# Kernel tuning notes

Hardware: AMD Instinct MI355X
Metric: run time of the kernel (lower is better)

## Reference

```python
import jax, jax.numpy as jnp
import numpy as np

EPS = 1e-6
N_HEADS = 16
KV_HEADS = 4
HEAD_DIM = 64
N_REP = N_HEADS // KV_HEADS
N_EXPERTS = 8
TOP_K = 2


def _rms_norm(x, w):
    return x * jax.lax.rsqrt(jnp.mean(x * x, axis=-1, keepdims=True) + EPS) * w


def _apply_rope(x, fc):
    # x: (B,T,H,D); fc: (T, D//2, 2) holding (cos, sin)
    B, T, H, D = x.shape
    xr = x.reshape(B, T, H, D // 2, 2)
    f = fc.reshape(1, T, 1, D // 2, 2)
    re = xr[..., 0] * f[..., 0] - xr[..., 1] * f[..., 1]
    im = xr[..., 1] * f[..., 0] + xr[..., 0] * f[..., 1]
    return jnp.stack([re, im], axis=-1).reshape(B, T, H, D)


def _silu(x):
    return x * jax.nn.sigmoid(x)


def setup_inputs():
    key = jax.random.key(0)
    ks = jax.random.split(key, 16)
    B, T, C = 4, 1024, 1024
    IE, IS = 1024, 2048  # expert_inter_dim, shared inter_dim
    s = 0.02
    x = jax.random.normal(ks[0], (B, T, C), jnp.float32)
    inv_freq = 1.0 / (10000.0 ** (np.arange(0, HEAD_DIM, 2, dtype=np.float32) / HEAD_DIM))
    ang = np.outer(np.arange(T, dtype=np.float32), inv_freq)
    freq_cis = jnp.asarray(np.stack([np.cos(ang), np.sin(ang)], axis=-1), jnp.float32)
    causal = np.tril(np.ones((T, T), dtype=bool))
    mask = jnp.asarray(np.where(causal, 0.0, -1e9), dtype=jnp.float32).reshape(1, 1, T, T)
    window = jnp.zeros((1, 1, T, T), jnp.float32)
    return {
        "x": x,
        "freq_cis": freq_cis,
        "mask": mask,
        "window": window,
        "norm1_w": jnp.ones((C,), jnp.float32),
        "wq": jax.random.normal(ks[1], (N_HEADS * HEAD_DIM, C), jnp.float32) * s,
        "wk": jax.random.normal(ks[2], (KV_HEADS * HEAD_DIM, C), jnp.float32) * s,
        "wv": jax.random.normal(ks[3], (KV_HEADS * HEAD_DIM, C), jnp.float32) * s,
        "wo": jax.random.normal(ks[4], (C, N_HEADS * HEAD_DIM), jnp.float32) * s,
        "norm2_w": jnp.ones((C,), jnp.float32),
        "gate_w": jax.random.normal(ks[5], (N_EXPERTS, C), jnp.float32) * s,
        "exp_w1": jax.random.normal(ks[6], (N_EXPERTS, IE, C), jnp.float32) * s,
        "exp_w2": jax.random.normal(ks[7], (N_EXPERTS, IE, C), jnp.float32) * s,
        "exp_wp": jax.random.normal(ks[8], (N_EXPERTS, C, IE), jnp.float32) * s,
        "sh_w1": jax.random.normal(ks[9], (IS, C), jnp.float32) * s,
        "sh_w2": jax.random.normal(ks[10], (IS, C), jnp.float32) * s,
        "sh_wp": jax.random.normal(ks[11], (C, IS), jnp.float32) * s,
        "start_pos": 0,
    }


def reference(x, freq_cis, mask, window, norm1_w, wq, wk, wv, wo, norm2_w,
              gate_w, exp_w1, exp_w2, exp_wp, sh_w1, sh_w2, sh_wp, start_pos):
    B, T, C = x.shape
    # ---- pre-norm attention (GQA, Global mask, eval: no dropout) ----
    xn = _rms_norm(x, norm1_w)
    q = (xn @ wq.T).reshape(B, T, N_HEADS, HEAD_DIM)
    k = (xn @ wk.T).reshape(B, T, KV_HEADS, HEAD_DIM)
    v = (xn @ wv.T).reshape(B, T, KV_HEADS, HEAD_DIM)
    q = _apply_rope(q, freq_cis)
    k = _apply_rope(k, freq_cis)
    k = jnp.repeat(k, N_REP, axis=2)  # (B,T,H,D)
    v = jnp.repeat(v, N_REP, axis=2)
    scale = 1.0 / np.sqrt(HEAD_DIM).astype(np.float32)
    att = jnp.einsum("bqhd,bkhd->bhqk", q, k) * scale + mask
    p = jax.nn.softmax(att, axis=-1)
    o = jnp.einsum("bhqk,bkhd->bqhd", p, v).reshape(B, T, C)
    x = x + o @ wo.T
    # ---- pre-norm MoE FFN ----
    xn2 = _rms_norm(x, norm2_w).reshape(-1, C)  # (N,C)
    scores = xn2 @ gate_w.T                      # gate logits, returned
    probs = jax.nn.softmax(scores, axis=-1)
    top_w, top_i = jax.lax.top_k(probs, TOP_K)   # (N,K)
    # dense combine weights (N,E): zero for non-selected experts
    wfull = jnp.sum(jax.nn.one_hot(top_i, N_EXPERTS, dtype=x.dtype) * top_w[..., None], axis=1)
    h = _silu(jnp.einsum("nc,eic->eni", xn2, exp_w1)) * jnp.einsum("nc,eic->eni", xn2, exp_w2)
    ye = jnp.einsum("eni,eci->enc", h, exp_wp)   # per-expert outputs
    y = jnp.einsum("ne,enc->nc", wfull, ye)      # routed combine
    z = (_silu(xn2 @ sh_w1.T) * (xn2 @ sh_w2.T)) @ sh_wp.T  # shared expert
    out = x + (y + z).reshape(B, T, C)
    return out, scores
```

## Files before the change

### kernel.cpp

```cpp
#include <hip/hip_runtime.h>


typedef __bf16 bf16_t;
typedef __bf16 bf16x8 __attribute__((ext_vector_type(8)));
typedef __bf16 bf16x4 __attribute__((ext_vector_type(4)));
typedef float  f32x4  __attribute__((ext_vector_type(4)));

#define GLD16(gp, lp) __builtin_amdgcn_global_load_lds(                         \
    (const __attribute__((address_space(1))) void*)(gp),                        \
    (__attribute__((address_space(3))) void*)(lp), 16, 0, 0)

__global__ __launch_bounds__(256) void convert_k(
    const float* __restrict__ src, bf16_t* __restrict__ dst)
{
    size_t i = (size_t)blockIdx.x * 256 + threadIdx.x;
    float4 v = *((const float4*)src + i);
    bf16x4 o;
    o[0] = (bf16_t)v.x; o[1] = (bf16_t)v.y; o[2] = (bf16_t)v.z; o[3] = (bf16_t)v.w;
    *((bf16x4*)dst + i) = o;
}

__global__ __launch_bounds__(256) void gemm_bt(
    const bf16_t* __restrict__ A, const bf16_t* __restrict__ W,
    int M, int N, int K, int ldw, int mode,
    float* __restrict__ outF, bf16_t* __restrict__ outB,
    const float* __restrict__ resF)
{
    __shared__ __align__(16) bf16_t sA[128 * 64];
    __shared__ __align__(16) bf16_t sB[128 * 64];
    const int tid  = threadIdx.x;
    const int bm   = blockIdx.y * 128, bn = blockIdx.x * 128;
    const int lane = tid & 63;
    const int wv   = tid >> 6;
    const int wm   = (wv >> 1) * 64, wn = (wv & 1) * 64;
    const int lr   = lane & 15;
    const int kg   = lane >> 4;

    f32x4 acc[4][4];
    #pragma unroll
    for (int i = 0; i < 4; ++i)
        #pragma unroll
        for (int j = 0; j < 4; ++j)
            acc[i][j] = f32x4{0.f, 0.f, 0.f, 0.f};

    for (int k0 = 0; k0 < K; k0 += 64) {
        #pragma unroll
        for (int p = 0; p < 4; ++p) {
            int idx = p * 256 + tid;
            int row = idx >> 3, ch = (idx & 7) * 8;
            GLD16(A + (size_t)(bm + row) * K   + k0 + ch, sA + idx * 8);
            GLD16(W + (size_t)(bn + row) * ldw + k0 + ch, sB + idx * 8);
        }
        __syncthreads();
        #pragma unroll
        for (int ks = 0; ks < 2; ++ks) {
            bf16x8 af[4], bfr[4];
            #pragma unroll
            for (int i = 0; i < 4; ++i)
                af[i] = *(const bf16x8*)(sA + (wm + i * 16 + lr) * 64 + ks * 32 + kg * 8);
            #pragma unroll
            for (int j = 0; j < 4; ++j)
                bfr[j] = *(const bf16x8*)(sB + (wn + j * 16 + lr) * 64 + ks * 32 + kg * 8);
            #pragma unroll
            for (int i = 0; i < 4; ++i)
                #pragma unroll
                for (int j = 0; j < 4; ++j)
                    acc[i][j] = __builtin_amdgcn_mfma_f32_16x16x32_bf16(
                        af[i], bfr[j], acc[i][j], 0, 0, 0);
        }
        __syncthreads();
    }

    #pragma unroll
    for (int i = 0; i < 4; ++i) {
        #pragma unroll
        for (int j = 0; j < 4; ++j) {
            #pragma unroll
            for (int rr = 0; rr < 4; ++rr) {
                int m = bm + wm + i * 16 + kg * 4 + rr;
                int n = bn + wn + j * 16 + lr;
                size_t o = (size_t)m * N + n;
                float v = acc[i][j][rr];
                if (mode == 0)      outF[o] = v;
                else if (mode == 1) outB[o] = (bf16_t)v;
                else                outF[o] = v + resF[o];
            }
        }
    }
}

__global__ __launch_bounds__(256) void gemm_glu(
    const bf16_t* __restrict__ A, const bf16_t* __restrict__ W1,
    const bf16_t* __restrict__ W2, int M, int N, int K,
    bf16_t* __restrict__ out)
{
    __shared__ __align__(16) bf16_t sA[128 * 64];
    __shared__ __align__(16) bf16_t sB1[128 * 64];
    __shared__ __align__(16) bf16_t sB2[128 * 64];
    const int tid  = threadIdx.x;
    const int bm   = blockIdx.y * 128, bn = blockIdx.x * 128;
    const int lane = tid & 63;
    const int wv   = tid >> 6;
    const int wm   = (wv >> 1) * 64, wn = (wv & 1) * 64;
    const int lr   = lane & 15;
    const int kg   = lane >> 4;

    f32x4 acc1[4][4], acc2[4][4];
    #pragma unroll
    for (int i = 0; i < 4; ++i)
        #pragma unroll
        for (int j = 0; j < 4; ++j) {
            acc1[i][j] = f32x4{0.f, 0.f, 0.f, 0.f};
            acc2[i][j] = f32x4{0.f, 0.f, 0.f, 0.f};
        }

    for (int k0 = 0; k0 < K; k0 += 64) {
        #pragma unroll
        for (int p = 0; p < 4; ++p) {
            int idx = p * 256 + tid;
            int row = idx >> 3, ch = (idx & 7) * 8;
            GLD16(A  + (size_t)(bm + row) * K + k0 + ch, sA  + idx * 8);
            GLD16(W1 + (size_t)(bn + row) * K + k0 + ch, sB1 + idx * 8);
            GLD16(W2 + (size_t)(bn + row) * K + k0 + ch, sB2 + idx * 8);
        }
        __syncthreads();
        #pragma unroll
        for (int ks = 0; ks < 2; ++ks) {
            bf16x8 af[4], b1[4], b2[4];
            #pragma unroll
            for (int i = 0; i < 4; ++i)
                af[i] = *(const bf16x8*)(sA + (wm + i * 16 + lr) * 64 + ks * 32 + kg * 8);
            #pragma unroll
            for (int j = 0; j < 4; ++j) {
                b1[j] = *(const bf16x8*)(sB1 + (wn + j * 16 + lr) * 64 + ks * 32 + kg * 8);
                b2[j] = *(const bf16x8*)(sB2 + (wn + j * 16 + lr) * 64 + ks * 32 + kg * 8);
            }
            #pragma unroll
            for (int i = 0; i < 4; ++i)
                #pragma unroll
                for (int j = 0; j < 4; ++j) {
                    acc1[i][j] = __builtin_amdgcn_mfma_f32_16x16x32_bf16(
                        af[i], b1[j], acc1[i][j], 0, 0, 0);
                    acc2[i][j] = __builtin_amdgcn_mfma_f32_16x16x32_bf16(
                        af[i], b2[j], acc2[i][j], 0, 0, 0);
                }
        }
        __syncthreads();
    }

    #pragma unroll
    for (int i = 0; i < 4; ++i) {
        #pragma unroll
        for (int j = 0; j < 4; ++j) {
            #pragma unroll
            for (int rr = 0; rr < 4; ++rr) {
                int m = bm + wm + i * 16 + kg * 4 + rr;
                int n = bn + wn + j * 16 + lr;
                float v1 = acc1[i][j][rr], v2 = acc2[i][j][rr];
                out[(size_t)m * N + n] = (bf16_t)(v1 / (1.f + __expf(-v1)) * v2);
            }
        }
    }
}

__global__ __launch_bounds__(256) void glu_gather(
    const bf16_t* __restrict__ A, const bf16_t* __restrict__ W1,
    const bf16_t* __restrict__ W2, const int* __restrict__ tok_list,
    const int* __restrict__ cnt, const int* __restrict__ off,
    bf16_t* __restrict__ h)
{
    const int e = blockIdx.y >> 5, t = blockIdx.y & 31;
    const int ce = cnt[e];
    if (t * 128 >= ce) return;
    const int hbase = off[e] + t * 128;
    const bf16_t* W1e = W1 + (size_t)e * 1048576;
    const bf16_t* W2e = W2 + (size_t)e * 1048576;

    __shared__ __align__(16) bf16_t sA[128 * 64];
    __shared__ __align__(16) bf16_t sB1[128 * 64];
    __shared__ __align__(16) bf16_t sB2[128 * 64];
    const int tid  = threadIdx.x;
    const int bn   = blockIdx.x * 128;
    const int lane = tid & 63;
    const int wv   = tid >> 6;
    const int wm   = (wv >> 1) * 64, wn = (wv & 1) * 64;
    const int lr   = lane & 15;
    const int kg   = lane >> 4;

    int tok4[4];
    #pragma unroll
    for (int p = 0; p < 4; ++p)
        tok4[p] = tok_list[e * 4096 + t * 128 + p * 32 + (tid >> 3)];

    f32x4 acc1[4][4], acc2[4][4];
    #pragma unroll
    for (int i = 0; i < 4; ++i)
        #pragma unroll
        for (int j = 0; j < 4; ++j) {
            acc1[i][j] = f32x4{0.f, 0.f, 0.f, 0.f};
            acc2[i][j] = f32x4{0.f, 0.f, 0.f, 0.f};
        }

    for (int k0 = 0; k0 < 1024; k0 += 64) {
        #pragma unroll
        for (int p = 0; p < 4; ++p) {
            int idx = p * 256 + tid;
            int row = idx >> 3, ch = (idx & 7) * 8;
            GLD16(A   + (size_t)tok4[p] * 1024 + k0 + ch, sA  + idx * 8);
            GLD16(W1e + (size_t)(bn + row) * 1024 + k0 + ch, sB1 + idx * 8);
            GLD16(W2e + (size_t)(bn + row) * 1024 + k0 + ch, sB2 + idx * 8);
        }
        __syncthreads();
        #pragma unroll
        for (int ks = 0; ks < 2; ++ks) {
            bf16x8 af[4], b1[4], b2[4];
            #pragma unroll
            for (int i = 0; i < 4; ++i)
                af[i] = *(const bf16x8*)(sA + (wm + i * 16 + lr) * 64 + ks * 32 + kg * 8);
            #pragma unroll
            for (int j = 0; j < 4; ++j) {
                b1[j] = *(const bf16x8*)(sB1 + (wn + j * 16 + lr) * 64 + ks * 32 + kg * 8);
                b2[j] = *(const bf16x8*)(sB2 + (wn + j * 16 + lr) * 64 + ks * 32 + kg * 8);
            }
            #pragma unroll
            for (int i = 0; i < 4; ++i)
                #pragma unroll
                for (int j = 0; j < 4; ++j) {
                    acc1[i][j] = __builtin_amdgcn_mfma_f32_16x16x32_bf16(
                        af[i], b1[j], acc1[i][j], 0, 0, 0);
                    acc2[i][j] = __builtin_amdgcn_mfma_f32_16x16x32_bf16(
                        af[i], b2[j], acc2[i][j], 0, 0, 0);
                }
        }
        __syncthreads();
    }

    #pragma unroll
    for (int i = 0; i < 4; ++i) {
        #pragma unroll
        for (int j = 0; j < 4; ++j) {
            #pragma unroll
            for (int rr = 0; rr < 4; ++rr) {
                int rl = wm + i * 16 + kg * 4 + rr;
                int n  = bn + wn + j * 16 + lr;
                float v1 = acc1[i][j][rr], v2 = acc2[i][j][rr];
                h[(size_t)(hbase + rl) * 1024 + n] =
                    (bf16_t)(v1 / (1.f + __expf(-v1)) * v2);
            }
        }
    }
}

__global__ __launch_bounds__(256) void down_gather(
    const bf16_t* __restrict__ h, const bf16_t* __restrict__ Wp,
    const int* __restrict__ tok_list, const float* __restrict__ w_list,
    const int* __restrict__ cnt, const int* __restrict__ off,
    float* __restrict__ y)
{
    const int e = blockIdx.y >> 5, t = blockIdx.y & 31;
    const int ce = cnt[e];
    if (t * 128 >= ce) return;
    const int hbase = off[e] + t * 128;
    const bf16_t* We = Wp + (size_t)e * 1048576;

    __shared__ __align__(16) bf16_t sA[128 * 64];
    __shared__ __align__(16) bf16_t sB[128 * 64];
    const int tid  = threadIdx.x;
    const int bn   = blockIdx.x * 128;
    const int lane = tid & 63;
    const int wv   = tid >> 6;
    const int wm   = (wv >> 1) * 64, wn = (wv & 1) * 64;
    const int lr   = lane & 15;
    const int kg   = lane >> 4;

    f32x4 acc[4][4];
    #pragma unroll
    for (int i = 0; i < 4; ++i)
        #pragma unroll
        for (int j = 0; j < 4; ++j)
            acc[i][j] = f32x4{0.f, 0.f, 0.f, 0.f};

    for (int k0 = 0; k0 < 1024; k0 += 64) {
        #pragma unroll
        for (int p = 0; p < 4; ++p) {
            int idx = p * 256 + tid;
            int row = idx >> 3, ch = (idx & 7) * 8;
            GLD16(h  + (size_t)(hbase + row) * 1024 + k0 + ch, sA + idx * 8);
            GLD16(We + (size_t)(bn + row) * 1024 + k0 + ch,    sB + idx * 8);
        }
        __syncthreads();
        #pragma unroll
        for (int ks = 0; ks < 2; ++ks) {
            bf16x8 af[4], bfr[4];
            #pragma unroll
            for (int i = 0; i < 4; ++i)
                af[i] = *(const bf16x8*)(sA + (wm + i * 16 + lr) * 64 + ks * 32 + kg * 8);
            #pragma unroll
            for (int j = 0; j < 4; ++j)
                bfr[j] = *(const bf16x8*)(sB + (wn + j * 16 + lr) * 64 + ks * 32 + kg * 8);
            #pragma unroll
            for (int i = 0; i < 4; ++i)
                #pragma unroll
                for (int j = 0; j < 4; ++j)
                    acc[i][j] = __builtin_amdgcn_mfma_f32_16x16x32_bf16(
                        af[i], bfr[j], acc[i][j], 0, 0, 0);
        }
        __syncthreads();
    }

    #pragma unroll
    for (int i = 0; i < 4; ++i) {
        #pragma unroll
        for (int rr = 0; rr < 4; ++rr) {
            int rl = t * 128 + wm + i * 16 + kg * 4 + rr;
            if (rl < ce) {
                int   tok = tok_list[e * 4096 + rl];
                float wgt = w_list[e * 4096 + rl];
                #pragma unroll
                for (int j = 0; j < 4; ++j) {
                    int n = bn + wn + j * 16 + lr;
                    atomicAdd(&y[(size_t)tok * 1024 + n], wgt * acc[i][j][rr]);
                }
            }
        }
    }
}

__global__ __launch_bounds__(256) void rmsnorm_k(
    const float* __restrict__ src, const float* __restrict__ w,
    bf16_t* __restrict__ dst)
{
    const int row = blockIdx.x, tid = threadIdx.x;
    float4 t4 = *((const float4*)src + (size_t)row * 256 + tid);
    float ssum = t4.x*t4.x + t4.y*t4.y + t4.z*t4.z + t4.w*t4.w;
    #pragma unroll
    for (int off = 32; off > 0; off >>= 1) ssum += __shfl_down(ssum, off);
    __shared__ float red[4];
    if ((tid & 63) == 0) red[tid >> 6] = ssum;
    __syncthreads();
    float total = red[0] + red[1] + red[2] + red[3];
    float rms = rsqrtf(total * (1.0f / 1024.0f) + 1e-6f);
    float4 w4 = *((const float4*)w + tid);
    bf16x4 o4;
    o4[0] = (bf16_t)(t4.x * rms * w4.x);
    o4[1] = (bf16_t)(t4.y * rms * w4.y);
    o4[2] = (bf16_t)(t4.z * rms * w4.z);
    o4[3] = (bf16_t)(t4.w * rms * w4.w);
    *((bf16x4*)dst + (size_t)row * 256 + tid) = o4;
}

__global__ __launch_bounds__(256) void rmsnorm_gate_k(
    const float* __restrict__ src, const float* __restrict__ w,
    const float* __restrict__ gw, bf16_t* __restrict__ dst,
    float* __restrict__ scores, int* __restrict__ topi,
    float* __restrict__ topw)
{
    const int row = blockIdx.x, tid = threadIdx.x;
    float4 t4 = *((const float4*)src + (size_t)row * 256 + tid);
    float ssum = t4.x*t4.x + t4.y*t4.y + t4.z*t4.z + t4.w*t4.w;
    #pragma unroll
    for (int off = 32; off > 0; off >>= 1) ssum += __shfl_down(ssum, off);
    __shared__ float red[4];
    if ((tid & 63) == 0) red[tid >> 6] = ssum;
    __syncthreads();
    float total = red[0] + red[1] + red[2] + red[3];
    float rms = rsqrtf(total * (1.0f / 1024.0f) + 1e-6f);
    float4 w4 = *((const float4*)w + tid);
    float4 f4;
    f4.x = t4.x * rms * w4.x;
    f4.y = t4.y * rms * w4.y;
    f4.z = t4.z * rms * w4.z;
    f4.w = t4.w * rms * w4.w;
    bf16x4 o4;
    o4[0] = (bf16_t)f4.x; o4[1] = (bf16_t)f4.y;
    o4[2] = (bf16_t)f4.z; o4[3] = (bf16_t)f4.w;
    *((bf16x4*)dst + (size_t)row * 256 + tid) = o4;

    float a[8];
    #pragma unroll
    for (int e = 0; e < 8; ++e) {
        float4 g4 = *((const float4*)(gw + (size_t)e * 1024) + tid);
        a[e] = f4.x * g4.x + f4.y * g4.y + f4.z * g4.z + f4.w * g4.w;
    }
    #pragma unroll
    for (int e = 0; e < 8; ++e)
        #pragma unroll
        for (int off = 32; off > 0; off >>= 1) a[e] += __shfl_down(a[e], off);
    __shared__ float gred[4][8];
    if ((tid & 63) == 0)
        #pragma unroll
        for (int e = 0; e < 8; ++e) gred[tid >> 6][e] = a[e];
    __syncthreads();
    if (tid == 0) {
        float lg[8];
        #pragma unroll
        for (int e = 0; e < 8; ++e)
            lg[e] = gred[0][e] + gred[1][e] + gred[2][e] + gred[3][e];
        #pragma unroll
        for (int e = 0; e < 8; ++e) scores[(size_t)row * 8 + e] = lg[e];
        float mx = lg[0];
        #pragma unroll
        for (int e = 1; e < 8; ++e) mx = fmaxf(mx, lg[e]);
        float p[8], sum = 0.f;
        #pragma unroll
        for (int e = 0; e < 8; ++e) { p[e] = __expf(lg[e] - mx); sum += p[e]; }
        float inv = 1.0f / sum;
        #pragma unroll
        for (int e = 0; e < 8; ++e) p[e] *= inv;
        int i1 = 0;
        #pragma unroll
        for (int e = 1; e < 8; ++e) if (p[e] > p[i1]) i1 = e;
        int i2 = (i1 == 0) ? 1 : 0;
        #pragma unroll
        for (int e = 0; e < 8; ++e) if (e != i1 && p[e] > p[i2]) i2 = e;
        topi[row] = i1 | (i2 << 8);
        topw[row * 2]     = p[i1];
        topw[row * 2 + 1] = p[i2];
    }
}

__global__ __launch_bounds__(256) void build_lists_k(
    const int* __restrict__ topi, const float* __restrict__ topw,
    int* __restrict__ tok_list, float* __restrict__ w_list,
    int* __restrict__ cnt)
{
    const int e = blockIdx.x;
    const int tid = threadIdx.x, lane = tid & 63, wv = tid >> 6;
    __shared__ int wc[4];
    int base = 0;
    for (int t0 = 0; t0 < 4096; t0 += 256) {
        int tok = t0 + tid;
        int ti = topi[tok];
        int i1 = ti & 255, i2 = (ti >> 8) & 255;
        bool m = (i1 == e) || (i2 == e);
        unsigned long long b = __ballot(m);
        if (lane == 0) wc[wv] = __popcll(b);
        __syncthreads();
        int pos = base;
        #pragma unroll
        for (int k = 0; k < 4; ++k) if (k < wv) pos += wc[k];
        pos += __popcll(b & ((1ull << lane) - 1ull));
        if (m) {
            tok_list[e * 4096 + pos] = tok;
            w_list[e * 4096 + pos]   = (i1 == e) ? topw[tok * 2] : topw[tok * 2 + 1];
        }
        base += wc[0] + wc[1] + wc[2] + wc[3];
        __syncthreads();
    }
    int padded = (base + 127) & ~127;
    for (int p = base + tid; p < padded; p += 256) tok_list[e * 4096 + p] = 0;
    if (tid == 0) cnt[e] = base;
}

__global__ void plan_k(const int* __restrict__ cnt, int* __restrict__ off)
{
    if (threadIdx.x == 0) {
        int run = 0;
        for (int e = 0; e < 8; ++e) {
            off[e] = run;
            run += (cnt[e] + 127) & ~127;
        }
    }
}

__global__ __launch_bounds__(256) void rope_k(
    bf16_t* __restrict__ buf, const float* __restrict__ fc, int nh)
{
    int idx = blockIdx.x * 256 + threadIdx.x;
    int pr = idx & 31;
    int hn = idx >> 5;
    int h  = hn % nh;
    int n  = hn / nh;
    int tpos = n & 1023;
    const float* f = fc + ((size_t)tpos * 32 + pr) * 2;
    float c = f[0], s = f[1];
    size_t base = ((size_t)n * nh + h) * 64 + pr * 2;
    float x0 = (float)buf[base], x1 = (float)buf[base + 1];
    buf[base]     = (bf16_t)(x0 * c - x1 * s);
    buf[base + 1] = (bf16_t)(x1 * c + x0 * s);
}

__global__ __launch_bounds__(256) void transpose_v(
    const bf16_t* __restrict__ vb, bf16_t* __restrict__ vt)
{
    __shared__ bf16_t tile[64][72];
    const int tt = blockIdx.x, kvh = blockIdx.y, b = blockIdx.z;
    const int tid = threadIdx.x;
    {
        int r = tid >> 2, c = (tid & 3) * 16;
        const bf16_t* src = vb + ((size_t)(b * 1024 + tt * 64 + r)) * 256 + kvh * 64 + c;
        bf16x8 v0 = *(const bf16x8*)src;
        bf16x8 v1 = *(const bf16x8*)(src + 8);
        *(bf16x8*)&tile[r][c] = v0;
        *(bf16x8*)&tile[r][c + 8] = v1;
    }
    __syncthreads();
    {
        int d = tid >> 2, t4 = (tid & 3) * 16;
        bf16_t* dst = vt + ((size_t)((b * 4 + kvh) * 64 + d)) * 1024 + tt * 64 + t4;
        bf16x8 o0, o1;
        #pragma unroll
        for (int u = 0; u < 8; ++u) {
            o0[u] = tile[t4 + u][d];
            o1[u] = tile[t4 + 8 + u][d];
        }
        *(bf16x8*)dst = o0;
        *(bf16x8*)(dst + 8) = o1;
    }
}

__global__ __launch_bounds__(256) void attn_mfma(
    const bf16_t* __restrict__ qb, const bf16_t* __restrict__ kb,
    const bf16_t* __restrict__ vt, bf16_t* __restrict__ ob)
{
    const int qt = blockIdx.x, h = blockIdx.y, b = blockIdx.z;
    const int kvh = h >> 2;
    __shared__ __align__(16) bf16_t sK[64 * 64];
    __shared__ __align__(16) bf16_t sVt[64 * 64];
    __shared__ __align__(16) bf16_t sP[64 * 72];
    const int tid  = threadIdx.x;
    const int w    = tid >> 6;
    const int lane = tid & 63;
    const int lr   = lane & 15;
    const int kg   = lane >> 4;

    bf16x8 qf[2];
    {
        const bf16_t* qrow = qb + ((size_t)(b * 1024 + qt * 64 + w * 16 + lr)) * 1024 + h * 64;
        qf[0] = *(const bf16x8*)(qrow + kg * 8);
        qf[1] = *(const bf16x8*)(qrow + 32 + kg * 8);
    }
    float m_run[4], l_run[4];
    f32x4 o_acc[4];
    #pragma unroll
    for (int rr = 0; rr < 4; ++rr) { m_run[rr] = -1.0e30f; l_run[rr] = 0.f; }
    #pragma unroll
    for (int dt = 0; dt < 4; ++dt) o_acc[dt] = f32x4{0.f, 0.f, 0.f, 0.f};

    for (int kt = 0; kt <= qt; ++kt) {
        #pragma unroll
        for (int p = 0; p < 2; ++p) {
            int idx = p * 256 + tid;
            int row = idx >> 3, ch = (idx & 7) * 8;
            GLD16(kb + ((size_t)(b * 1024 + kt * 64 + row)) * 256 + kvh * 64 + ch,
                  sK + idx * 8);
            GLD16(vt + ((size_t)((b * 4 + kvh) * 64 + row)) * 1024 + kt * 64 + ch,
                  sVt + idx * 8);
        }
        __syncthreads();

        f32x4 sfr[4];
        #pragma unroll
        for (int j = 0; j < 4; ++j) {
            sfr[j] = f32x4{0.f, 0.f, 0.f, 0.f};
            #pragma unroll
            for (int ks = 0; ks < 2; ++ks) {
                bf16x8 bf = *(const bf16x8*)(sK + (j * 16 + lr) * 64 + ks * 32 + kg * 8);
                sfr[j] = __builtin_amdgcn_mfma_f32_16x16x32_bf16(qf[ks], bf, sfr[j], 0, 0, 0);
            }
        }
        const int rowg = qt * 64 + w * 16 + kg * 4;
        float mnew[4];
        #pragma unroll
        for (int rr = 0; rr < 4; ++rr) mnew[rr] = m_run[rr];
        #pragma unroll
        for (int j = 0; j < 4; ++j) {
            int colg = kt * 64 + j * 16 + lr;
            #pragma unroll
            for (int rr = 0; rr < 4; ++rr) {
                float s = sfr[j][rr] * 0.125f;
                if (colg > rowg + rr) s = -1.0e30f;
                sfr[j][rr] = s;
                mnew[rr] = fmaxf(mnew[rr], s);
            }
        }
        #pragma unroll
        for (int off = 1; off < 16; off <<= 1)
            #pragma unroll
            for (int rr = 0; rr < 4; ++rr)
                mnew[rr] = fmaxf(mnew[rr], __shfl_xor(mnew[rr], off, 64));
        float alpha[4], lpart[4];
        #pragma unroll
        for (int rr = 0; rr < 4; ++rr) {
            alpha[rr] = __expf(m_run[rr] - mnew[rr]);
            lpart[rr] = 0.f;
        }
        #pragma unroll
        for (int j = 0; j < 4; ++j)
            #pragma unroll
            for (int rr = 0; rr < 4; ++rr) {
                float p = __expf(sfr[j][rr] - mnew[rr]);
                sfr[j][rr] = p;
                lpart[rr] += p;
            }
        #pragma unroll
        for (int j = 0; j < 4; ++j)
            #pragma unroll
            for (int rr = 0; rr < 4; ++rr)
                sP[(w * 16 + kg * 4 + rr) * 72 + j * 16 + lr] = (bf16_t)sfr[j][rr];
        #pragma unroll
        for (int off = 1; off < 16; off <<= 1)
            #pragma unroll
            for (int rr = 0; rr < 4; ++rr)
                lpart[rr] += __shfl_xor(lpart[rr], off, 64);
        #pragma unroll
        for (int rr = 0; rr < 4; ++rr) {
            l_run[rr] = l_run[rr] * alpha[rr] + lpart[rr];
            m_run[rr] = mnew[rr];
        }
        #pragma unroll
        for (int dt = 0; dt < 4; ++dt)
            #pragma unroll
            for (int rr = 0; rr < 4; ++rr)
                o_acc[dt][rr] *= alpha[rr];
        #pragma unroll
        for (int ks = 0; ks < 2; ++ks) {
            bf16x8 af = *(const bf16x8*)(sP + (w * 16 + lr) * 72 + ks * 32 + kg * 8);
            #pragma unroll
            for (int dt = 0; dt < 4; ++dt) {
                bf16x8 bf = *(const bf16x8*)(sVt + (dt * 16 + lr) * 64 + ks * 32 + kg * 8);
                o_acc[dt] = __builtin_amdgcn_mfma_f32_16x16x32_bf16(af, bf, o_acc[dt], 0, 0, 0);
            }
        }
        __syncthreads();
    }

    float inv[4];
    #pragma unroll
    for (int rr = 0; rr < 4; ++rr) inv[rr] = 1.0f / l_run[rr];
    #pragma unroll
    for (int dt = 0; dt < 4; ++dt)
        #pragma unroll
        for (int rr = 0; rr < 4; ++rr) {
            int tok = qt * 64 + w * 16 + kg * 4 + rr;
            ob[((size_t)(b * 1024 + tok)) * 1024 + h * 64 + dt * 16 + lr] =
                (bf16_t)(o_acc[dt][rr] * inv[rr]);
        }
}

__global__ __launch_bounds__(256) void finalize_k(
    const float* __restrict__ x1, const float* __restrict__ y, float* __restrict__ out)
{
    size_t i = (size_t)blockIdx.x * 256 + threadIdx.x;
    float4 a = *((const float4*)x1 + i);
    float4 b = *((const float4*)y + i);
    float4 o4;
    o4.x = a.x + b.x; o4.y = a.y + b.y; o4.z = a.z + b.z; o4.w = a.w + b.w;
    *((float4*)out + i) = o4;
}

extern "C" void kernel_launch(void* const* d_in, const int* in_sizes, int n_in,
                              void* d_out, int out_size, void* d_ws, size_t ws_size,
                              hipStream_t stream)
{
    const float* x   = (const float*)d_in[0];
    const float* fc  = (const float*)d_in[1];
    const float* n1w = (const float*)d_in[4];
    const float* wq  = (const float*)d_in[5];
    const float* wk  = (const float*)d_in[6];
    const float* wv  = (const float*)d_in[7];
    const float* wo  = (const float*)d_in[8];
    const float* n2w = (const float*)d_in[9];
    const float* gw  = (const float*)d_in[10];
    const float* ew1 = (const float*)d_in[11];
    const float* ew2 = (const float*)d_in[12];
    const float* ewp = (const float*)d_in[13];
    const float* sw1 = (const float*)d_in[14];
    const float* sw2 = (const float*)d_in[15];
    const float* swp = (const float*)d_in[16];

    const size_t MB = 1024 * 1024;
    char* ws = (char*)d_ws;
    bf16_t* xnb  = (bf16_t*)(ws + 0);
    float*  x1   = (float*) (ws + 8 * MB);
    float*  y    = (float*) (ws + 24 * MB);
    char*   slotA= ws + 40 * MB;
    bf16_t* h    = (bf16_t*)(ws + 56 * MB);
    char*   lists= ws + 74 * MB;
    int*    tok_list = (int*)lists;
    float*  w_list   = (float*)(lists + 131072);
    int*    cnt      = (int*)(lists + 262144);
    int*    off      = (int*)(lists + 262208);
    int*    topi     = (int*)(lists + 262400);
    float*  topw     = (float*)(lists + 278784);
    bf16_t* qb   = (bf16_t*)(ws + 75 * MB);
    bf16_t* kb   = (bf16_t*)(ws + 83 * MB);
    bf16_t* vb   = (bf16_t*)(ws + 85 * MB);
    bf16_t* ob   = (bf16_t*)(ws + 87 * MB);
    bf16_t* vt   = (bf16_t*)(ws + 95 * MB);

    float* outp   = (float*)d_out;
    float* scores = outp + (size_t)4096 * 1024;

    auto conv = [&](const float* s, bf16_t* d, size_t cntN) {
        convert_k<<<cntN / 1024, 256, 0, stream>>>(s, d);
    };
    auto gemm = [&](const bf16_t* A, const bf16_t* W, int M, int N, int K, int ldw,
                    int mode, float* oF, bf16_t* oB, const float* res) {
        gemm_bt<<<dim3(N / 128, M / 128), 256, 0, stream>>>(
            A, W, M, N, K, ldw, mode, oF, oB, res);
    };
    auto glu = [&](const bf16_t* A, const bf16_t* W1, const bf16_t* W2,
                   int M, int N, int K, bf16_t* o) {
        gemm_glu<<<dim3(N / 128, M / 128), 256, 0, stream>>>(A, W1, W2, M, N, K, o);
    };

    bf16_t* wqb = (bf16_t*)slotA;
    bf16_t* wkb = wqb + 1048576;
    bf16_t* wvb = wkb + 262144;
    bf16_t* wob = wvb + 262144;
    conv(wq, wqb, 1048576);
    conv(wk, wkb, 262144);
    conv(wv, wvb, 262144);
    conv(wo, wob, 1048576);

    rmsnorm_k<<<4096, 256, 0, stream>>>(x, n1w, xnb);
    gemm(xnb, wqb, 4096, 1024, 1024, 1024, 1, nullptr, qb, nullptr);
    gemm(xnb, wkb, 4096, 256, 1024, 1024, 1, nullptr, kb, nullptr);
    gemm(xnb, wvb, 4096, 256, 1024, 1024, 1, nullptr, vb, nullptr);
    rope_k<<<(4096 * 16 * 32) / 256, 256, 0, stream>>>(qb, fc, 16);
    rope_k<<<(4096 * 4 * 32) / 256, 256, 0, stream>>>(kb, fc, 4);
    transpose_v<<<dim3(16, 4, 4), 256, 0, stream>>>(vb, vt);
    attn_mfma<<<dim3(16, 16, 4), 256, 0, stream>>>(qb, kb, vt, ob);
    gemm(ob, wob, 4096, 1024, 1024, 1024, 2, x1, nullptr, x);

    rmsnorm_gate_k<<<4096, 256, 0, stream>>>(x1, n2w, gw, xnb, scores, topi, topw);
    build_lists_k<<<8, 256, 0, stream>>>(topi, topw, tok_list, w_list, cnt);
    plan_k<<<1, 64, 0, stream>>>(cnt, off);

    bf16_t* sw1b = (bf16_t*)(ws + 75 * MB);
    bf16_t* sw2b = sw1b + 2097152;
    bf16_t* swpb = sw2b + 2097152;
    conv(sw1, sw1b, 2097152);
    conv(sw2, sw2b, 2097152);
    conv(swp, swpb, 2097152);
    bf16_t* hb = (bf16_t*)slotA;
    glu(xnb, sw1b, sw2b, 4096, 2048, 1024, hb);
    gemm(hb, swpb, 4096, 1024, 2048, 2048, 0, y, nullptr, nullptr);

    bf16_t* ew1b = (bf16_t*)slotA;
    bf16_t* ew2b = (bf16_t*)(ws + 75 * MB);
    conv(ew1, ew1b, 8388608);
    conv(ew2, ew2b, 8388608);
    glu_gather<<<dim3(8, 256), 256, 0, stream>>>(xnb, ew1b, ew2b,
                                                 tok_list, cnt, off, h);
    bf16_t* ewpb = (bf16_t*)slotA;
    conv(ewp, ewpb, 8388608);
    down_gather<<<dim3(8, 256), 256, 0, stream>>>(h, ewpb,
                                                  tok_list, w_list, cnt, off, y);

    finalize_k<<<(4096 * 1024) / 1024, 256, 0, stream>>>(x1, y, outp);
    (void)in_sizes; (void)n_in; (void)out_size; (void)ws_size;
}
```

Baseline: 740.7 us.

## Fuse QKV projection, batch weight conversions, accumulate MoE outputs directly into output

Merges the Q/K/V projections into one GEMM over a packed QKV buffer and applies RoPE to Q and K in one kernel. Weight conversions are batched into multi-segment launches, and the plan and finalize kernels are removed by computing segment offsets inline and accumulating shared and routed expert outputs directly into the output. It also adds an XOR swizzle for K/V tiles in attention LDS to reduce bank conflicts. The risk lies in workspace aliasing and reliance on launch ordering.

```diff
diff --git a/kernel.cpp b/kernel.cpp
--- a/kernel.cpp
+++ b/kernel.cpp
@@ -5,6 +5,8 @@
 typedef __bf16 bf16x8 __attribute__((ext_vector_type(8)));
 typedef __bf16 bf16x4 __attribute__((ext_vector_type(4)));
 typedef float  f32x4  __attribute__((ext_vector_type(4)));
+
+#define LQKV 1536
 
 #define GLD16(gp, lp) __builtin_amdgcn_global_load_lds(                         \
     (const __attribute__((address_space(1))) void*)(gp),                        \
@@ -20,11 +22,30 @@
     *((bf16x4*)dst + i) = o;
 }
 
+struct Cvt8 {
+    const float* s[8];
+    bf16_t* d[8];
+    int cum[9];
+    int nseg;
+};
+
+__global__ __launch_bounds__(256) void convert_multi_k(Cvt8 j)
+{
+    int blk = blockIdx.x;
+    int seg = 0;
+    while (seg + 1 < j.nseg && blk >= j.cum[seg + 1]) ++seg;
+    size_t i = (size_t)(blk - j.cum[seg]) * 256 + threadIdx.x;
+    float4 v = *((const float4*)j.s[seg] + i);
+    bf16x4 o;
+    o[0] = (bf16_t)v.x; o[1] = (bf16_t)v.y; o[2] = (bf16_t)v.z; o[3] = (bf16_t)v.w;
+    *((bf16x4*)j.d[seg] + i) = o;
+}
+
 __global__ __launch_bounds__(256) void gemm_bt(
     const bf16_t* __restrict__ A, const bf16_t* __restrict__ W,
     int M, int N, int K, int ldw, int mode,
     float* __restrict__ outF, bf16_t* __restrict__ outB,
-    const float* __restrict__ resF)
+    const float* __restrict__ resF, float* __restrict__ outF2)
 {
     __shared__ __align__(16) bf16_t sA[128 * 64];
     __shared__ __align__(16) bf16_t sB[128 * 64];
@@ -83,7 +104,11 @@
                 float v = acc[i][j][rr];
                 if (mode == 0)      outF[o] = v;
                 else if (mode == 1) outB[o] = (bf16_t)v;
-                else                outF[o] = v + resF[o];
+                else if (mode == 2) {
+                    float r = v + resF[o];
+                    outF[o] = r;
+                    if (outF2) outF2[o] = r;
+                } else              outF[o] += v;
             }
         }
     }
@@ -163,16 +188,23 @@
     }
 }
 
+__device__ __forceinline__ int seg_off(const int* cnt, int e)
+{
+    int r = 0;
+    #pragma unroll
+    for (int k = 0; k < 8; ++k) if (k < e) r += (cnt[k] + 127) & ~127;
+    return r;
+}
+
 __global__ __launch_bounds__(256) void glu_gather(
     const bf16_t* __restrict__ A, const bf16_t* __restrict__ W1,
     const bf16_t* __restrict__ W2, const int* __restrict__ tok_list,
-    const int* __restrict__ cnt, const int* __restrict__ off,
-    bf16_t* __restrict__ h)
+    const int* __restrict__ cnt, bf16_t* __restrict__ h)
 {
     const int e = blockIdx.y >> 5, t = blockIdx.y & 31;
     const int ce = cnt[e];
     if (t * 128 >= ce) return;
-    const int hbase = off[e] + t * 128;
+    const int hbase = seg_off(cnt, e) + t * 128;
     const bf16_t* W1e = W1 + (size_t)e * 1048576;
     const bf16_t* W2e = W2 + (size_t)e * 1048576;
 
@@ -190,7 +222,7 @@
     int tok4[4];
     #pragma unroll
     for (int p = 0; p < 4; ++p)
-        tok4[p] = tok_list[e * 4096 + t * 128 + p * 32 + (tid >> 3)];
+        tok4[p] = tok_list[e * 4096 + t * 128 + ((p * 256 + tid) >> 3)];
 
     f32x4 acc1[4][4], acc2[4][4];
     #pragma unroll
@@ -206,7 +238,7 @@
         for (int p = 0; p < 4; ++p) {
             int idx = p * 256 + tid;
             int row = idx >> 3, ch = (idx & 7) * 8;
-            GLD16(A   + (size_t)tok4[p] * 1024 + k0 + ch, sA  + idx * 8);
+            GLD16(A   + (size_t)tok4[p] * 1024 + k0 + ch,    sA  + idx * 8);
             GLD16(W1e + (size_t)(bn + row) * 1024 + k0 + ch, sB1 + idx * 8);
             GLD16(W2e + (size_t)(bn + row) * 1024 + k0 + ch, sB2 + idx * 8);
         }
@@ -254,13 +286,12 @@
 __global__ __launch_bounds__(256) void down_gather(
     const bf16_t* __restrict__ h, const bf16_t* __restrict__ Wp,
     const int* __restrict__ tok_list, const float* __restrict__ w_list,
-    const int* __restrict__ cnt, const int* __restrict__ off,
-    float* __restrict__ y)
+    const int* __restrict__ cnt, float* __restrict__ out)
 {
     const int e = blockIdx.y >> 5, t = blockIdx.y & 31;
     const int ce = cnt[e];
     if (t * 128 >= ce) return;
-    const int hbase = off[e] + t * 128;
+    const int hbase = seg_off(cnt, e) + t * 128;
     const bf16_t* We = Wp + (size_t)e * 1048576;
 
     __shared__ __align__(16) bf16_t sA[128 * 64];
@@ -312,14 +343,14 @@
     for (int i = 0; i < 4; ++i) {
         #pragma unroll
         for (int rr = 0; rr < 4; ++rr) {
-            int rl = t * 128 + wm + i * 16 + kg * 4 + rr;
-            if (rl < ce) {
-                int   tok = tok_list[e * 4096 + rl];
-                float wgt = w_list[e * 4096 + rl];
+            int g = t * 128 + wm + i * 16 + kg * 4 + rr;
+            if (g < ce) {
+                int   tok = tok_list[e * 4096 + g];
+                float wgt = w_list[e * 4096 + g];
                 #pragma unroll
                 for (int j = 0; j < 4; ++j) {
                     int n = bn + wn + j * 16 + lr;
-                    atomicAdd(&y[(size_t)tok * 1024 + n], wgt * acc[i][j][rr]);
+                    atomicAdd(&out[(size_t)tok * 1024 + n], wgt * acc[i][j][rr]);
                 }
             }
         }
@@ -452,43 +483,34 @@
     if (tid == 0) cnt[e] = base;
 }
 
-__global__ void plan_k(const int* __restrict__ cnt, int* __restrict__ off)
-{
-    if (threadIdx.x == 0) {
-        int run = 0;
-        for (int e = 0; e < 8; ++e) {
-            off[e] = run;
-            run += (cnt[e] + 127) & ~127;
-        }
-    }
-}
-
-__global__ __launch_bounds__(256) void rope_k(
-    bf16_t* __restrict__ buf, const float* __restrict__ fc, int nh)
+__global__ __launch_bounds__(256) void rope_all_k(
+    bf16_t* __restrict__ qkv, const float* __restrict__ fc)
 {
     int idx = blockIdx.x * 256 + threadIdx.x;
     int pr = idx & 31;
     int hn = idx >> 5;
-    int h  = hn % nh;
-    int n  = hn / nh;
+    int h  = hn % 20;
+    int n  = hn / 20;
     int tpos = n & 1023;
     const float* f = fc + ((size_t)tpos * 32 + pr) * 2;
     float c = f[0], s = f[1];
-    size_t base = ((size_t)n * nh + h) * 64 + pr * 2;
-    float x0 = (float)buf[base], x1 = (float)buf[base + 1];
-    buf[base]     = (bf16_t)(x0 * c - x1 * s);
-    buf[base + 1] = (bf16_t)(x1 * c + x0 * s);
+    int col = (h < 16) ? h * 64 : 1024 + (h - 16) * 64;
+    size_t base = (size_t)n * LQKV + col + pr * 2;
+    float x0 = (float)qkv[base], x1 = (float)qkv[base + 1];
+    qkv[base]     = (bf16_t)(x0 * c - x1 * s);
+    qkv[base + 1] = (bf16_t)(x1 * c + x0 * s);
 }
 
 __global__ __launch_bounds__(256) void transpose_v(
-    const bf16_t* __restrict__ vb, bf16_t* __restrict__ vt)
+    const bf16_t* __restrict__ qkv, bf16_t* __restrict__ vt)
 {
     __shared__ bf16_t tile[64][72];
     const int tt = blockIdx.x, kvh = blockIdx.y, b = blockIdx.z;
     const int tid = threadIdx.x;
     {
         int r = tid >> 2, c = (tid & 3) * 16;
-        const bf16_t* src = vb + ((size_t)(b * 1024 + tt * 64 + r)) * 256 + kvh * 64 + c;
+        const bf16_t* src = qkv + ((size_t)(b * 1024 + tt * 64 + r)) * LQKV
+                            + 1280 + kvh * 64 + c;
         bf16x8 v0 = *(const bf16x8*)src;
         bf16x8 v1 = *(const bf16x8*)(src + 8);
         *(bf16x8*)&tile[r][c] = v0;
@@ -510,8 +532,8 @@
 }
 
 __global__ __launch_bounds__(256) void attn_mfma(
-    const bf16_t* __restrict__ qb, const bf16_t* __restrict__ kb,
-    const bf16_t* __restrict__ vt, bf16_t* __restrict__ ob)
+    const bf16_t* __restrict__ qkv, const bf16_t* __restrict__ vt,
+    bf16_t* __restrict__ ob)
 {
     const int qt = blockIdx.x, h = blockIdx.y, b = blockIdx.z;
     const int kvh = h >> 2;
@@ -523,10 +545,12 @@
     const int lane = tid & 63;
     const int lr   = lane & 15;
     const int kg   = lane >> 4;
+    const int swz  = (lr & 7) << 3;
 
     bf16x8 qf[2];
     {
-        const bf16_t* qrow = qb + ((size_t)(b * 1024 + qt * 64 + w * 16 + lr)) * 1024 + h * 64;
+        const bf16_t* qrow = qkv + ((size_t)(b * 1024 + qt * 64 + w * 16 + lr)) * LQKV
+                             + h * 64;
         qf[0] = *(const bf16x8*)(qrow + kg * 8);
         qf[1] = *(const bf16x8*)(qrow + 32 + kg * 8);
     }
@@ -541,10 +565,11 @@
         #pragma unroll
         for (int p = 0; p < 2; ++p) {
             int idx = p * 256 + tid;
-            int row = idx >> 3, ch = (idx & 7) * 8;
-            GLD16(kb + ((size_t)(b * 1024 + kt * 64 + row)) * 256 + kvh * 64 + ch,
-                  sK + idx * 8);
-            GLD16(vt + ((size_t)((b * 4 + kvh) * 64 + row)) * 1024 + kt * 64 + ch,
+            int row = idx >> 3;
+            int chs = ((idx & 7) * 8) ^ ((row & 7) << 3);
+            GLD16(qkv + ((size_t)(b * 1024 + kt * 64 + row)) * LQKV
+                      + 1024 + kvh * 64 + chs, sK + idx * 8);
+            GLD16(vt + ((size_t)((b * 4 + kvh) * 64 + row)) * 1024 + kt * 64 + chs,
                   sVt + idx * 8);
         }
         __syncthreads();
@@ -555,7 +580,8 @@
             sfr[j] = f32x4{0.f, 0.f, 0.f, 0.f};
             #pragma unroll
             for (int ks = 0; ks < 2; ++ks) {
-                bf16x8 bf = *(const bf16x8*)(sK + (j * 16 + lr) * 64 + ks * 32 + kg * 8);
+                bf16x8 bf = *(const bf16x8*)(sK + (j * 16 + lr) * 64 +
+                                             ((ks * 32 + kg * 8) ^ swz));
                 sfr[j] = __builtin_amdgcn_mfma_f32_16x16x32_bf16(qf[ks], bf, sfr[j], 0, 0, 0);
             }
         }
@@ -618,7 +644,8 @@
             bf16x8 af = *(const bf16x8*)(sP + (w * 16 + lr) * 72 + ks * 32 + kg * 8);
             #pragma unroll
             for (int dt = 0; dt < 4; ++dt) {
-                bf16x8 bf = *(const bf16x8*)(sVt + (dt * 16 + lr) * 64 + ks * 32 + kg * 8);
+                bf16x8 bf = *(const bf16x8*)(sVt + (dt * 16 + lr) * 64 +
+                                             ((ks * 32 + kg * 8) ^ swz));
                 o_acc[dt] = __builtin_amdgcn_mfma_f32_16x16x32_bf16(af, bf, o_acc[dt], 0, 0, 0);
             }
         }
@@ -636,17 +663,6 @@
             ob[((size_t)(b * 1024 + tok)) * 1024 + h * 64 + dt * 16 + lr] =
                 (bf16_t)(o_acc[dt][rr] * inv[rr]);
         }
-}
-
-__global__ __launch_bounds__(256) void finalize_k(
-    const float* __restrict__ x1, const float* __restrict__ y, float* __restrict__ out)
-{
-    size_t i = (size_t)blockIdx.x * 256 + threadIdx.x;
-    float4 a = *((const float4*)x1 + i);
-    float4 b = *((const float4*)y + i);
-    float4 o4;
-    o4.x = a.x + b.x; o4.y = a.y + b.y; o4.z = a.z + b.z; o4.w = a.w + b.w;
-    *((float4*)out + i) = o4;
 }
 
 extern "C" void kernel_launch(void* const* d_in, const int* in_sizes, int n_in,
@@ -673,82 +689,79 @@
     char* ws = (char*)d_ws;
     bf16_t* xnb  = (bf16_t*)(ws + 0);
     float*  x1   = (float*) (ws + 8 * MB);
-    float*  y    = (float*) (ws + 24 * MB);
-    char*   slotA= ws + 40 * MB;
-    bf16_t* h    = (bf16_t*)(ws + 56 * MB);
-    char*   lists= ws + 74 * MB;
+    bf16_t* ew2b = (bf16_t*)(ws + 8 * MB);
+    bf16_t* h    = (bf16_t*)(ws + 24 * MB);
+    char*   lists= ws + 42 * MB;
     int*    tok_list = (int*)lists;
     float*  w_list   = (float*)(lists + 131072);
     int*    cnt      = (int*)(lists + 262144);
-    int*    off      = (int*)(lists + 262208);
     int*    topi     = (int*)(lists + 262400);
     float*  topw     = (float*)(lists + 278784);
-    bf16_t* qb   = (bf16_t*)(ws + 75 * MB);
-    bf16_t* kb   = (bf16_t*)(ws + 83 * MB);
-    bf16_t* vb   = (bf16_t*)(ws + 85 * MB);
-    bf16_t* ob   = (bf16_t*)(ws + 87 * MB);
-    bf16_t* vt   = (bf16_t*)(ws + 95 * MB);
+    bf16_t* sw1b = (bf16_t*)(ws + 43 * MB);
+    bf16_t* sw2b = (bf16_t*)(ws + 47 * MB);
+    bf16_t* swpb = (bf16_t*)(ws + 51 * MB);
+    char*   slotA= ws + 55 * MB;
+    bf16_t* hb   = (bf16_t*)slotA;
+    bf16_t* qkv  = (bf16_t*)(ws + 71 * MB);
+    bf16_t* ob   = (bf16_t*)(ws + 83 * MB);
+    bf16_t* vt   = (bf16_t*)(ws + 91 * MB);
+    bf16_t* ew1b = (bf16_t*)(ws + 71 * MB);
+    bf16_t* ewpb = (bf16_t*)(ws + 71 * MB);
 
     float* outp   = (float*)d_out;
     float* scores = outp + (size_t)4096 * 1024;
 
-    auto conv = [&](const float* s, bf16_t* d, size_t cntN) {
-        convert_k<<<cntN / 1024, 256, 0, stream>>>(s, d);
-    };
     auto gemm = [&](const bf16_t* A, const bf16_t* W, int M, int N, int K, int ldw,
-                    int mode, float* oF, bf16_t* oB, const float* res) {
+                    int mode, float* oF, bf16_t* oB, const float* res, float* oF2) {
         gemm_bt<<<dim3(N / 128, M / 128), 256, 0, stream>>>(
-            A, W, M, N, K, ldw, mode, oF, oB, res);
-    };
-    auto glu = [&](const bf16_t* A, const bf16_t* W1, const bf16_t* W2,
-                   int M, int N, int K, bf16_t* o) {
-        gemm_glu<<<dim3(N / 128, M / 128), 256, 0, stream>>>(A, W1, W2, M, N, K, o);
+            A, W, M, N, K, ldw, mode, oF, oB, res, oF2);
     };
 
     bf16_t* wqb = (bf16_t*)slotA;
     bf16_t* wkb = wqb + 1048576;
     bf16_t* wvb = wkb + 262144;
     bf16_t* wob = wvb + 262144;
-    conv(wq, wqb, 1048576);
-    conv(wk, wkb, 262144);
-    conv(wv, wvb, 262144);
-    conv(wo, wob, 1048576);
+    {
+        Cvt8 j;
+        j.s[0]=wq;  j.d[0]=wqb;  j.s[1]=wk;  j.d[1]=wkb;
+        j.s[2]=wv;  j.d[2]=wvb;  j.s[3]=wo;  j.d[3]=wob;
+        j.s[4]=sw1; j.d[4]=sw1b; j.s[5]=sw2; j.d[5]=sw2b;
+        j.s[6]=swp; j.d[6]=swpb; j.s[7]=nullptr; j.d[7]=nullptr;
+        int sz[7] = {1024, 256, 256, 1024, 2048, 2048, 2048};
+        j.cum[0] = 0;
+        for (int k = 0; k < 7; ++k) j.cum[k + 1] = j.cum[k] + sz[k];
+        j.cum[8] = j.cum[7];
+        j.nseg = 7;
+        convert_multi_k<<<j.cum[7], 256, 0, stream>>>(j);
+    }
 
     rmsnorm_k<<<4096, 256, 0, stream>>>(x, n1w, xnb);
-    gemm(xnb, wqb, 4096, 1024, 1024, 1024, 1, nullptr, qb, nullptr);
-    gemm(xnb, wkb, 4096, 256, 1024, 1024, 1, nullptr, kb, nullptr);
-    gemm(xnb, wvb, 4096, 256, 1024, 1024, 1, nullptr, vb, nullptr);
-    rope_k<<<(4096 * 16 * 32) / 256, 256, 0, stream>>>(qb, fc, 16);
-    rope_k<<<(4096 * 4 * 32) / 256, 256, 0, stream>>>(kb, fc, 4);
-    transpose_v<<<dim3(16, 4, 4), 256, 0, stream>>>(vb, vt);
-    attn_mfma<<<dim3(16, 16, 4), 256, 0, stream>>>(qb, kb, vt, ob);
-    gemm(ob, wob, 4096, 1024, 1024, 1024, 2, x1, nullptr, x);
+    gemm(xnb, wqb, 4096, LQKV, 1024, 1024, 1, nullptr, qkv, nullptr, nullptr);
+    rope_all_k<<<(4096 * 20 * 32) / 256, 256, 0, stream>>>(qkv, fc);
+    transpose_v<<<dim3(16, 4, 4), 256, 0, stream>>>(qkv, vt);
+    attn_mfma<<<dim3(16, 16, 4), 256, 0, stream>>>(qkv, vt, ob);
+    gemm(ob, wob, 4096, 1024, 1024, 1024, 2, x1, nullptr, x, outp);
 
     rmsnorm_gate_k<<<4096, 256, 0, stream>>>(x1, n2w, gw, xnb, scores, topi, topw);
     build_lists_k<<<8, 256, 0, stream>>>(topi, topw, tok_list, w_list, cnt);
-    plan_k<<<1, 64, 0, stream>>>(cnt, off);
-
-    bf16_t* sw1b = (bf16_t*)(ws + 75 * MB);
-    bf16_t* sw2b = sw1b + 2097152;
-    bf16_t* swpb = sw2b + 2097152;
-    conv(sw1, sw1b, 2097152);
-    conv(sw2, sw2b, 2097152);
-    conv(swp, swpb, 2097152);
-    bf16_t* hb = (bf16_t*)slotA;
-    glu(xnb, sw1b, sw2b, 4096, 2048, 1024, hb);
-    gemm(hb, swpb, 4096, 1024, 2048, 2048, 0, y, nullptr, nullptr);
-
-    bf16_t* ew1b = (bf16_t*)slotA;
-    bf16_t* ew2b = (bf16_t*)(ws + 75 * MB);
-    conv(ew1, ew1b, 8388608);
-    conv(ew2, ew2b, 8388608);
-    glu_gather<<<dim3(8, 256), 256, 0, stream>>>(xnb, ew1b, ew2b,
-                                                 tok_list, cnt, off, h);
-    bf16_t* ewpb = (bf16_t*)slotA;
-    conv(ewp, ewpb, 8388608);
-    down_gather<<<dim3(8, 256), 256, 0, stream>>>(h, ewpb,
-                                                  tok_list, w_list, cnt, off, y);
-
-    finalize_k<<<(4096 * 1024) / 1024, 256, 0, stream>>>(x1, y, outp);
+
+    {
+        Cvt8 j;
+        j.s[0]=ew1; j.d[0]=ew1b; j.s[1]=ew2; j.d[1]=ew2b;
+        for (int k = 2; k < 8; ++k) { j.s[k]=nullptr; j.d[k]=nullptr; }
+        j.cum[0] = 0; j.cum[1] = 8192; j.cum[2] = 16384;
+        for (int k = 3; k < 9; ++k) j.cum[k] = 16384;
+        j.nseg = 2;
+        convert_multi_k<<<16384, 256, 0, stream>>>(j);
+    }
+
+    gemm_glu<<<dim3(16, 32), 256, 0, stream>>>(xnb, sw1b, sw2b, 4096, 2048, 1024, hb);
+    glu_gather<<<dim3(8, 256), 256, 0, stream>>>(xnb, ew1b, ew2b, tok_list, cnt, h);
+
+    convert_k<<<8192, 256, 0, stream>>>(ewp, ewpb);
+
+    gemm(hb, swpb, 4096, 1024, 2048, 2048, 3, outp, nullptr, nullptr, nullptr);
+    down_gather<<<dim3(8, 256), 256, 0, stream>>>(h, ewpb, tok_list, w_list, cnt, outp);
+
     (void)in_sizes; (void)n_in; (void)out_size; (void)ws_size;
 }
```

Measured after the change: 675.1 us. 1.1x faster.
